# Performance work log

Hardware: AMD Instinct MI355X
Metric: run time of the kernel (lower is better)

## Reference

```python
import jax, jax.numpy as jnp
import numpy as np

K = 3
OUT_H, OUT_W = 32, 512
INVALID_DIST = 1e10  # stands in for filtering out zero points on the reference side


def _downsample(pc, out_H=OUT_H, out_W=OUT_W):
    # pc: [B, H, W, 3] -> [B, out_H, out_W, 3] via strided index selection
    B, H, W, _ = pc.shape
    sH, sW = H // out_H, W // out_W
    return pc[:, : out_H * sH : sH, : out_W * sW : sW, :]


def _batch_knn_mean(tgt, src):
    # tgt: [Nt, 3] reference points; src: [Ns, 3] query points.
    # move_zero_point filters points whose xyz are all zero; with fixed shapes we
    # emulate this by masking: invalid refs get huge distance (never selected in
    # top-k unless all refs invalid), invalid queries are excluded from the mean.
    valid_t = jnp.any(tgt != 0.0, axis=-1)  # [Nt]
    valid_s = jnp.any(src != 0.0, axis=-1)  # [Ns]
    # pairwise squared Euclidean distance [Ns, Nt]
    d2 = (
        jnp.sum(src * src, axis=-1)[:, None]
        + jnp.sum(tgt * tgt, axis=-1)[None, :]
        - 2.0 * (src @ tgt.T)
    )
    d = jnp.sqrt(jnp.maximum(d2, 0.0))  # KNN_CUDA returns Euclidean distance
    d = jnp.where(valid_t[None, :], d, INVALID_DIST)
    neg_topk, _ = jax.lax.top_k(-d, K)  # k smallest distances per query
    dk = -neg_topk  # [Ns, K]
    w = valid_s.astype(d.dtype)
    denom = K * jnp.maximum(jnp.sum(w), 1.0)
    return jnp.sum(dk * w[:, None]) / denom  # mean over valid query knn dists


def reference(source_pc, target_pc):
    # source_pc: [B, H, W, 3]; target_pc: [B, 3, H, W]
    B = source_pc.shape[0]
    tgt = _downsample(jnp.transpose(target_pc, (0, 2, 3, 1))).reshape(B, -1, 3)
    src = _downsample(source_pc).reshape(B, -1, 3)
    per_batch = jax.vmap(_batch_knn_mean)(tgt, src)  # [B]
    return jnp.mean(per_batch)


def setup_inputs() -> dict:
    key = jax.random.key(0)
    k1, k2 = jax.random.split(key)
    source_pc = jax.random.normal(k1, (2, 64, 2048, 3), dtype=jnp.float32)
    target_pc = jax.random.normal(k2, (2, 3, 64, 2048), dtype=jnp.float32)
    return {"source_pc": source_pc, "target_pc": target_pc}
```

## Files before the change

kernel.cpp:

```cpp
#include <hip/hip_runtime.h>
#include <math.h>

#define NB 2
#define NQ 16384
#define IN_H 64
#define IN_W 2048
#define BIG 1e30f
#define NQT (NB * NQ)
#define NG 8
#define NP (NG * 3)

typedef __bf16 bf16x8 __attribute__((ext_vector_type(8)));
typedef float f32x16 __attribute__((ext_vector_type(16)));

__device__ inline float med3(float a, float b, float c) {
    return __builtin_amdgcn_fmed3f(a, b, c);
}
#define INSERT3(B0, B1, B2, V)                    \
    do { float _v = (V);                          \
         (B2) = med3((B1), (B2), _v);             \
         (B1) = med3((B0), (B1), _v);             \
         (B0) = fminf((B0), _v); } while (0)

union PK { __bf16 h[8]; uint4 u; };

__global__ __launch_bounds__(256) void pack_kernel(
    const float* __restrict__ tgt_pc,
    uint4* __restrict__ packed,
    float4* __restrict__ tgt4,
    float* __restrict__ zws)
{
    if (blockIdx.x == 0 && threadIdx.x < 16) zws[threadIdx.x] = 0.f;

    int gid = blockIdx.x * 256 + threadIdx.x;
    int b = gid >> 14, t = gid & (NQ - 1);
    int oh = t >> 9, ow = t & 511;
    const size_t PL = (size_t)IN_H * IN_W;
    size_t base = ((size_t)(b * 3) * IN_H + oh * 2) * IN_W + ow * 4;
    float x = tgt_pc[base], y = tgt_pc[base + PL], z = tgt_pc[base + 2 * PL];
    bool valid = (x != 0.f) || (y != 0.f) || (z != 0.f);
    float ntx = x * x + y * y + z * z;
    float nt = valid ? ntx : BIG;
    float tx = valid ? -2.f * x : 0.f;
    float ty = valid ? -2.f * y : 0.f;
    float tz = valid ? -2.f * z : 0.f;

    __bf16 txh = (__bf16)tx, tyh = (__bf16)ty, tzh = (__bf16)tz;
    __bf16 txl = (__bf16)(tx - (float)txh);
    __bf16 tyl = (__bf16)(ty - (float)tyh);
    __bf16 tzl = (__bf16)(tz - (float)tzh);
    __bf16 nth = (__bf16)nt;
    __bf16 ntl = (__bf16)(nt - (float)nth);

    PK h0, h1;
    h0.h[0] = txh; h0.h[1] = tyh; h0.h[2] = tzh; h0.h[3] = txh;
    h0.h[4] = tyh; h0.h[5] = tzh; h0.h[6] = txl; h0.h[7] = tyl;
    h1.h[0] = tzl; h1.h[1] = nth; h1.h[2] = ntl; h1.h[3] = (__bf16)1.0f;
    h1.h[4] = (__bf16)1.0f; h1.h[5] = (__bf16)0.0f;
    h1.h[6] = (__bf16)0.0f; h1.h[7] = (__bf16)0.0f;

    int tile = t >> 5, m = t & 31;
    size_t o = (size_t)(b * 512 + tile) * 64 + m;
    packed[o]      = h0.u;
    packed[o + 32] = h1.u;

    tgt4[gid] = make_float4(valid ? x : 0.f, valid ? y : 0.f,
                            valid ? z : 0.f, valid ? ntx : 1e20f);
}

__global__ __launch_bounds__(256, 6) void knn_mfma(
    const float* __restrict__ src_pc,
    const uint4* __restrict__ packed,
    const float4* __restrict__ tgt4,
    float* __restrict__ partial)
{
    __shared__ uint4 lds[2][512];
    const int tid = threadIdx.x;
    const int lane = tid & 63;
    const int w = tid >> 6;
    int blk = blockIdx.x;
    int qt = blk & 127;
    int e8 = (blk >> 7) & 7;
    int b = blk >> 10;

    int n = lane & 31;
    int q = qt * 128 + w * 32 + n;
    size_t sbase = (((size_t)b * IN_H + (q >> 9) * 2) * IN_W + (q & 511) * 4) * 3;
    float sx = src_pc[sbase], sy = src_pc[sbase + 1], sz = src_pc[sbase + 2];
    float ns = sx * sx + sy * sy + sz * sz;
    __bf16 sxh = (__bf16)sx, syh = (__bf16)sy, szh = (__bf16)sz;
    __bf16 sxl = (__bf16)(sx - (float)sxh);
    __bf16 syl = (__bf16)(sy - (float)syh);
    __bf16 szl = (__bf16)(sz - (float)szh);
    __bf16 nsh = (__bf16)ns;
    __bf16 nsl = (__bf16)(ns - (float)nsh);
    bf16x8 bq;
    if ((lane >> 5) == 0) {
        bq[0] = sxh; bq[1] = syh; bq[2] = szh; bq[3] = sxl;
        bq[4] = syl; bq[5] = szl; bq[6] = sxh; bq[7] = syh;
    } else {
        bq[0] = szh; bq[1] = (__bf16)1.0f; bq[2] = (__bf16)1.0f; bq[3] = nsh;
        bq[4] = nsl; bq[5] = (__bf16)0.0f; bq[6] = (__bf16)0.0f; bq[7] = (__bf16)0.0f;
    }

    f32x16 zero;
    #pragma unroll
    for (int i = 0; i < 16; ++i) zero[i] = 0.f;

    float c0 = BIG, c1 = BIG, c2 = BIG;

    const uint4* pkq = packed + (size_t)b * 32768 + (size_t)e8 * 4096;

    uint4 r[2];
    r[0] = pkq[tid]; r[1] = pkq[tid + 256];
    lds[0][tid] = r[0]; lds[0][tid + 256] = r[1];
    __syncthreads();

    for (int c = 0; c < 8; ++c) {
        int cur = c & 1;
        uint4 rn[2];
        if (c < 7) {
            const uint4* s = pkq + (c + 1) * 512;
            rn[0] = s[tid]; rn[1] = s[tid + 256];
        }
        const uint4* buf = lds[cur];
        #pragma unroll 2
        for (int t = 0; t < 8; ++t) {
            bf16x8 af = __builtin_bit_cast(bf16x8, buf[t * 64 + lane]);
            f32x16 d = __builtin_amdgcn_mfma_f32_32x32x16_bf16(af, bq, zero, 0, 0, 0);
            float m0 = fminf(fminf(d[0], d[1]), fminf(d[2], d[3]));
            float m1 = fminf(fminf(d[4], d[5]), fminf(d[6], d[7]));
            float m2 = fminf(fminf(d[8], d[9]), fminf(d[10], d[11]));
            float m3 = fminf(fminf(d[12], d[13]), fminf(d[14], d[15]));
            float m = fminf(fminf(m0, m1), fminf(m2, m3));
            unsigned u = (__float_as_uint(m) & ~63u) | (unsigned)(c * 8 + t);
            float pv = __uint_as_float(u);
            INSERT3(c0, c1, c2, pv);
        }
        if (c < 7) {
            lds[1 - cur][tid] = rn[0];
            lds[1 - cur][tid + 256] = rn[1];
        }
        __syncthreads();
    }

    int half = lane >> 5;
    int ti[3] = { (int)(__float_as_uint(c0) & 63u),
                  (int)(__float_as_uint(c1) & 63u),
                  (int)(__float_as_uint(c2) & 63u) };
    float e0 = BIG, e1 = BIG, e2 = BIG;
    const float4* t4b = tgt4 + (size_t)b * NQ + (size_t)e8 * 2048;
    #pragma unroll
    for (int i = 0; i < 3; ++i) {
        int tbase = ti[i] * 32 + 4 * half;
        #pragma unroll
        for (int rr = 0; rr < 16; ++rr) {
            int row = (rr & 3) + 8 * (rr >> 2);
            float4 t4 = t4b[tbase + row];
            float dot = sx * t4.x;
            dot = fmaf(sy, t4.y, dot);
            dot = fmaf(sz, t4.z, dot);
            float d2 = fmaf(-2.f, dot, ns + t4.w);
            INSERT3(e0, e1, e2, d2);
        }
    }

    float f0 = __shfl_down(e0, 32, 64);
    float f1 = __shfl_down(e1, 32, 64);
    float f2 = __shfl_down(e2, 32, 64);
    if (lane < 32) {
        INSERT3(e0, e1, e2, f0);
        INSERT3(e0, e1, e2, f1);
        INSERT3(e0, e1, e2, f2);
        int gq = b * NQ + q;
        partial[(e8 * 3 + 0) * NQT + gq] = e0;
        partial[(e8 * 3 + 1) * NQT + gq] = e1;
        partial[(e8 * 3 + 2) * NQT + gq] = e2;
    }
}

__global__ __launch_bounds__(256) void merge_final(
    const float* __restrict__ partial,
    const float* __restrict__ src_pc,
    float* __restrict__ accum,
    int* __restrict__ done_cnt,
    float* __restrict__ out)
{
    int gid = blockIdx.x * 256 + threadIdx.x;
    int b = gid >> 14;
    int q = gid & (NQ - 1);

    float b0 = BIG, b1 = BIG, b2 = BIG;
    #pragma unroll
    for (int c = 0; c < NP; ++c) {
        float v = partial[c * NQT + gid];
        INSERT3(b0, b1, b2, v);
    }

    size_t base = (((size_t)b * IN_H + (q >> 9) * 2) * IN_W + (q & 511) * 4) * 3;
    float x = src_pc[base], y = src_pc[base + 1], z = src_pc[base + 2];
    float wt = ((x != 0.f) || (y != 0.f) || (z != 0.f)) ? 1.f : 0.f;

    float d = fminf(sqrtf(fmaxf(b0, 0.f)), 1e10f)
            + fminf(sqrtf(fmaxf(b1, 0.f)), 1e10f)
            + fminf(sqrtf(fmaxf(b2, 0.f)), 1e10f);
    float dsum = d * wt;

    #pragma unroll
    for (int off = 32; off > 0; off >>= 1) {
        dsum += __shfl_down(dsum, off, 64);
        wt   += __shfl_down(wt, off, 64);
    }
    __shared__ float sd[4], sw4[4];
    int lane = threadIdx.x & 63, wv = threadIdx.x >> 6;
    if (lane == 0) { sd[wv] = dsum; sw4[wv] = wt; }
    __syncthreads();
    if (threadIdx.x == 0) {
        atomicAdd(&accum[b * 2 + 0], sd[0] + sd[1] + sd[2] + sd[3]);
        atomicAdd(&accum[b * 2 + 1], sw4[0] + sw4[1] + sw4[2] + sw4[3]);
        __threadfence();
        int done = atomicAdd(done_cnt, 1);
        if (done == (int)gridDim.x - 1) {
            float s0 = atomicAdd(&accum[0], 0.f);
            float c0 = atomicAdd(&accum[1], 0.f);
            float s1 = atomicAdd(&accum[2], 0.f);
            float c1 = atomicAdd(&accum[3], 0.f);
            float r = s0 / (3.0f * fmaxf(c0, 1.0f))
                    + s1 / (3.0f * fmaxf(c1, 1.0f));
            out[0] = r / (float)NB;
        }
    }
}

extern "C" void kernel_launch(void* const* d_in, const int* in_sizes, int n_in,
                              void* d_out, int out_size, void* d_ws, size_t ws_size,
                              hipStream_t stream) {
    const float* src_pc = (const float*)d_in[0];
    const float* tgt_pc = (const float*)d_in[1];
    float* out = (float*)d_out;

    char* ws = (char*)d_ws;
    float*  accum   = (float*)ws;
    int*    done    = (int*)(ws + 32);
    float*  partial = (float*)(ws + 64);
    uint4*  packed  = (uint4*)(ws + 3145792);
    float4* tgt4    = (float4*)(ws + 4194368);

    pack_kernel<<<NQT / 256, 256, 0, stream>>>(tgt_pc, packed, tgt4, (float*)ws);
    knn_mfma<<<NB * NG * 128, 256, 0, stream>>>(src_pc, packed, tgt4, partial);
    merge_final<<<NQT / 256, 256, 0, stream>>>(partial, src_pc, accum, done, out);
}
```

Measured before the change: 133.1 us.

## Load packed target tiles directly into registers, drop LDS staging and barriers

Each wave now reads its packed bf16 target tiles straight from global memory into registers, double-buffered four tiles at a time, instead of staging them through a shared LDS double buffer with block-wide syncs. The top-3 insertion is split into two independent chains merged at the end, to shorten the serial med3 dependency. This removes LDS traffic and __syncthreads, but each of the four waves now fetches the same tiles on its own, which relies on L1/L2 hits and raises register pressure.

```diff
diff --git a/kernel.cpp b/kernel.cpp
--- a/kernel.cpp
+++ b/kernel.cpp
@@ -74,7 +74,6 @@
     const float4* __restrict__ tgt4,
     float* __restrict__ partial)
 {
-    __shared__ uint4 lds[2][512];
     const int tid = threadIdx.x;
     const int lane = tid & 63;
     const int w = tid >> 6;
@@ -107,47 +106,48 @@
     #pragma unroll
     for (int i = 0; i < 16; ++i) zero[i] = 0.f;
 
-    float c0 = BIG, c1 = BIG, c2 = BIG;
-
-    const uint4* pkq = packed + (size_t)b * 32768 + (size_t)e8 * 4096;
-
-    uint4 r[2];
-    r[0] = pkq[tid]; r[1] = pkq[tid + 256];
-    lds[0][tid] = r[0]; lds[0][tid + 256] = r[1];
-    __syncthreads();
-
-    for (int c = 0; c < 8; ++c) {
-        int cur = c & 1;
-        uint4 rn[2];
-        if (c < 7) {
-            const uint4* s = pkq + (c + 1) * 512;
-            rn[0] = s[tid]; rn[1] = s[tid + 256];
-        }
-        const uint4* buf = lds[cur];
-        #pragma unroll 2
-        for (int t = 0; t < 8; ++t) {
-            bf16x8 af = __builtin_bit_cast(bf16x8, buf[t * 64 + lane]);
+    float c0a = BIG, c1a = BIG, c2a = BIG;
+    float c0b = BIG, c1b = BIG, c2b = BIG;
+
+    const uint4* pkq = packed + (size_t)b * 32768 + (size_t)e8 * 4096 + lane;
+
+    uint4 cur[4];
+    #pragma unroll
+    for (int i = 0; i < 4; ++i) cur[i] = pkq[i * 64];
+
+    for (int tt = 0; tt < 64; tt += 4) {
+        uint4 nxt[4];
+        if (tt + 4 < 64) {
+            #pragma unroll
+            for (int i = 0; i < 4; ++i) nxt[i] = pkq[(tt + 4 + i) * 64];
+        }
+        #pragma unroll
+        for (int i = 0; i < 4; ++i) {
+            bf16x8 af = __builtin_bit_cast(bf16x8, cur[i]);
             f32x16 d = __builtin_amdgcn_mfma_f32_32x32x16_bf16(af, bq, zero, 0, 0, 0);
             float m0 = fminf(fminf(d[0], d[1]), fminf(d[2], d[3]));
             float m1 = fminf(fminf(d[4], d[5]), fminf(d[6], d[7]));
             float m2 = fminf(fminf(d[8], d[9]), fminf(d[10], d[11]));
             float m3 = fminf(fminf(d[12], d[13]), fminf(d[14], d[15]));
             float m = fminf(fminf(m0, m1), fminf(m2, m3));
-            unsigned u = (__float_as_uint(m) & ~63u) | (unsigned)(c * 8 + t);
+            unsigned u = (__float_as_uint(m) & ~63u) | (unsigned)(tt + i);
             float pv = __uint_as_float(u);
-            INSERT3(c0, c1, c2, pv);
-        }
-        if (c < 7) {
-            lds[1 - cur][tid] = rn[0];
-            lds[1 - cur][tid + 256] = rn[1];
-        }
-        __syncthreads();
-    }
+            if (i & 1) { INSERT3(c0b, c1b, c2b, pv); }
+            else       { INSERT3(c0a, c1a, c2a, pv); }
+        }
+        if (tt + 4 < 64) {
+            #pragma unroll
+            for (int i = 0; i < 4; ++i) cur[i] = nxt[i];
+        }
+    }
+    INSERT3(c0a, c1a, c2a, c0b);
+    INSERT3(c0a, c1a, c2a, c1b);
+    INSERT3(c0a, c1a, c2a, c2b);
 
     int half = lane >> 5;
-    int ti[3] = { (int)(__float_as_uint(c0) & 63u),
-                  (int)(__float_as_uint(c1) & 63u),
-                  (int)(__float_as_uint(c2) & 63u) };
+    int ti[3] = { (int)(__float_as_uint(c0a) & 63u),
+                  (int)(__float_as_uint(c1a) & 63u),
+                  (int)(__float_as_uint(c2a) & 63u) };
     float e0 = BIG, e1 = BIG, e2 = BIG;
     const float4* t4b = tgt4 + (size_t)b * NQ + (size_t)e8 * 2048;
     #pragma unroll
```

New measurement: 135.4 us. Within noise of the previous version (+1.7%).
